# Kernel optimization log

Measured on AMD Instinct MI355X. Metric: run time of the kernel, lower is better.

Reference implementation:

```python
import jax, jax.numpy as jnp
import numpy as np

B, F, V, D = 16384, 16, 100000, 16  # batch, n_fields, vocab, embed_dim; dims = F*D = 256
EPS = 1e-5


def _bn(x, g, b):
    # torch.nn.BatchNorm1d in training mode: biased batch variance
    m = x.mean(0)
    v = x.var(0)
    return g * (x - m) * jax.lax.rsqrt(v + EPS) + b


def setup_inputs() -> dict:
    ks = iter(jax.random.split(jax.random.key(0), 40))

    def rn(shape, s=0.05):
        return jax.random.normal(next(ks), shape, jnp.float32) * s

    return {
        "feat_ids": jax.random.randint(next(ks), (B, F), 0, V, jnp.int32),
        "domain_ids": jax.random.randint(next(ks), (B,), 0, 3, jnp.int32),
        "emb": rn((F, V, D), 0.1),
        "hW0": rn((256, 128)), "hb0": jnp.zeros(128), "hg0": jnp.ones(128), "hbe0": jnp.zeros(128),
        "hW1": rn((128, 64)), "hb1": jnp.zeros(64), "hg1": jnp.ones(64), "hbe1": jnp.zeros(64),
        "hW2": rn((64, 1024)), "hb2": jnp.zeros(1024), "hg2": jnp.ones(1024), "hbe2": jnp.zeros(1024),
        "cw": rn((3, 256)), "cb": jnp.zeros((3, 256)),
        "mW0": rn((256, 512)), "mb0": jnp.zeros(512), "mg0": jnp.ones(512), "mbe0": jnp.zeros(512),
        "mW1": rn((512, 256)), "mb1": jnp.zeros(256), "mg1": jnp.ones(256), "mbe1": jnp.zeros(256),
        "u0": rn((256, 32)), "u1": rn((32, 32)), "v0": rn((32, 32)), "v1": rn((32, 256)),
        "ab0": jnp.zeros(32), "ab1": jnp.zeros(256),
        "gamma1": jnp.ones(256), "bias1": jnp.zeros(256),
        "lw": rn((512,)), "lb": jnp.zeros(1),
    }


def _forward(feat_ids, emb, hW0, hb0, hg0, hbe0, hW1, hb1, hg1, hbe1,
             hW2, hb2, hg2, hbe2, cw, cb, mW0, mb0, mg0, mbe0,
             mW1, mb1, mg1, mbe1, u0, u1, v0, v1, ab0, ab1,
             gamma1, bias1, lw, lb):
    b, f = feat_ids.shape
    # EmbeddingLayer(squeeze_dim=True): per-field lookup then concat -> [B, F*D]
    e = emb[jnp.arange(f)[None, :], feat_ids].reshape(b, -1)
    h = e
    for W, bb, g, be in ((hW0, hb0, hg0, hbe0), (hW1, hb1, hg1, hbe1), (hW2, hb2, hg2, hbe2)):
        h = jax.nn.relu(_bn(h @ W + bb, g, be))
    k = u1.shape[0]
    H = h.reshape(b, k, k)  # [B, k, k]
    # CrossNetwork: x_{l+1} = x0 * (x_l . w_l) + b_l + x_l
    x = e
    for i in range(cw.shape[0]):
        x = e * (x @ cw[i])[:, None] + cb[i] + x
    cn_out = x  # [B, 256]
    m = e
    for W, bb, g, be in ((mW0, mb0, mg0, mbe0), (mW1, mb1, mg1, mbe1)):
        m = jax.nn.relu(_bn(m @ W + bb, g, be))
    # hyper low-rank adapter: einsum('mi,bij,jn->bmn') applied lazily so the
    # [B,256,32] per-sample weight is never materialized (associativity)
    t = jax.nn.sigmoid(jnp.einsum('bi,bij->bj', m @ u0, H) @ v0 + ab0)   # [B, 32]
    t = jnp.einsum('bi,bij->bj', t @ u1, H) @ v1 + ab1                    # [B, 256]
    mu = t.mean(0)
    var = t.var(0, ddof=1)  # torch.var default is unbiased
    m = gamma1 * (t - mu) / jnp.sqrt(var + EPS) + bias1 + m  # norm + residual
    y = jnp.concatenate([cn_out, m], axis=1) @ lw + lb[0]     # LR head
    # Every domain branch computes identical values (shared weights, full-batch
    # input, dropout p=0), so the torch.where domain-select is the identity.
    return jax.nn.sigmoid(y)  # [B]


def reference(feat_ids, domain_ids, emb, hW0, hb0, hg0, hbe0, hW1, hb1, hg1, hbe1,
              hW2, hb2, hg2, hbe2, cw, cb, mW0, mb0, mg0, mbe0,
              mW1, mb1, mg1, mbe1, u0, u1, v0, v1, ab0, ab1,
              gamma1, bias1, lw, lb):
    return _forward(feat_ids, emb, hW0, hb0, hg0, hbe0, hW1, hb1, hg1, hbe1,
                    hW2, hb2, hg2, hbe2, cw, cb, mW0, mb0, mg0, mbe0,
                    mW1, mb1, mg1, mbe1, u0, u1, v0, v1, ab0, ab1,
                    gamma1, bias1, lw, lb)
```

## Files before the change

kernel.cpp:

```cpp
#include <hip/hip_runtime.h>

typedef unsigned short u16;
typedef __attribute__((ext_vector_type(8))) short bf16x8;
typedef __attribute__((ext_vector_type(4))) float f32x4;
#define BATCH 16384

__device__ __forceinline__ float b2f(u16 u){ unsigned int i=((unsigned int)u)<<16; float f; __builtin_memcpy(&f,&i,4); return f; }
__device__ __forceinline__ u16 f2b(float f){ unsigned int x; __builtin_memcpy(&x,&f,4); unsigned int r=(x + 0x7fffu + ((x>>16)&1u))>>16; return (u16)r; }

__global__ __launch_bounds__(256) void prep_kernel(float* __restrict__ S,
                                                   const float* __restrict__ hb0, const float* __restrict__ mb0,
                                                   float* __restrict__ catb,
                                                   const float* __restrict__ w0, const float* __restrict__ w1,
                                                   const float* __restrict__ w2, const float* __restrict__ w3,
                                                   const float* __restrict__ w4, const float* __restrict__ w5,
                                                   const float* __restrict__ w6,
                                                   u16* __restrict__ catWt, u16* __restrict__ t1,
                                                   u16* __restrict__ t2, u16* __restrict__ t4,
                                                   u16* __restrict__ t5, u16* __restrict__ t6,
                                                   const int* __restrict__ ids,
                                                   const float* __restrict__ emb,
                                                   u16* __restrict__ e){
  int blk = blockIdx.x;
  int tid = threadIdx.x;
  if (blk < 18){
    int i = blk*256 + tid;
    if (i < 4480) S[i] = 0.f;
  } else if (blk == 18){
    for (int i = tid; i < 640; i += 256) catb[i] = (i < 128) ? hb0[i] : mb0[i-128];
  } else if (blk < 1523){
    int c = blk - 19;
    if (c < 640){        int idx=c*256+tid;        int n=idx>>8, k=idx&255;
                         catWt[idx] = f2b(n<128 ? w0[k*128+n] : w3[k*512+(n-128)]); }
    else if (c < 672){   int idx=(c-640)*256+tid;  t1[idx]=f2b(w1[(idx%128)*64   + idx/128]); }
    else if (c < 928){   int idx=(c-672)*256+tid;  t2[idx]=f2b(w2[(idx%64)*1024  + idx/64]);  }
    else if (c < 1440){  int idx=(c-928)*256+tid;  t4[idx]=f2b(w4[(idx%512)*256  + idx/512]); }
    else if (c < 1472){  int idx=(c-1440)*256+tid; t5[idx]=f2b(w5[(idx%256)*32   + idx/256]); }
    else {               int idx=(c-1472)*256+tid; t6[idx]=f2b(w6[(idx%32)*256   + idx/32]);  }
  } else {
    int g = blk - 1523;
    int b = g*16 + (tid >> 4), f = tid & 15;
    int id = ids[b*16 + f];
    const float4* src = (const float4*)(emb + ((size_t)f*100000 + (size_t)id)*16);
    float4 v0 = src[0], v1 = src[1], v2 = src[2], v3 = src[3];
    u16 o[16] = { f2b(v0.x),f2b(v0.y),f2b(v0.z),f2b(v0.w), f2b(v1.x),f2b(v1.y),f2b(v1.z),f2b(v1.w),
                  f2b(v2.x),f2b(v2.y),f2b(v2.z),f2b(v2.w), f2b(v3.x),f2b(v3.y),f2b(v3.z),f2b(v3.w) };
    uint4 p0, p1; __builtin_memcpy(&p0, &o[0], 16); __builtin_memcpy(&p1, &o[8], 16);
    uint4* dst = (uint4*)(e + (size_t)b*256 + f*16);
    dst[0] = p0; dst[1] = p1;
  }
}

template<int BK>
__device__ __forceinline__ void gemm_body(const u16* __restrict__ A,
                                          const u16* __restrict__ Wt,
                                          const float* __restrict__ bias,
                                          u16* __restrict__ Ca,
                                          u16* __restrict__ Cb,
                                          int Nsplit,
                                          const float* __restrict__ asums,
                                          const float* __restrict__ asumsq,
                                          const float* __restrict__ ag,
                                          const float* __restrict__ abe,
                                          float* __restrict__ sums,
                                          float* __restrict__ sumsq,
                                          int N, int K, int n0, int m0,
                                          u16* lds, float* bnS, float* bnB){
  constexpr int STR = BK + 8;
  constexpr int EPT = BK/4;
  u16* As = lds;
  u16* Bs = lds + 64*STR;
  int tid = threadIdx.x;
  int lane = tid & 63, w = tid >> 6, quad = lane >> 4, m16 = lane & 15;
  int srow = tid >> 2, skoff = (tid & 3)*EPT;
  if (asums != nullptr){
    for (int k = tid; k < K; k += 256){
      float mean = asums[k] * (1.f/(float)BATCH);
      float var  = asumsq[k] * (1.f/(float)BATCH) - mean*mean;
      float sc   = ag[k] * rsqrtf(var + 1e-5f);
      bnS[k] = sc;
      bnB[k] = abe[k] - mean*sc;
    }
    __syncthreads();
  }
  f32x4 acc[4] = {};
  int ng = n0 + srow;
  uint4 a0, a1, b0, b1;
  {
    const u16* ap = A + (size_t)(m0+srow)*K + skoff;
    a0 = *(const uint4*)ap;
    if (EPT == 16) a1 = *(const uint4*)(ap + 8);
    if (ng < N){
      const u16* bp = Wt + (size_t)ng*K + skoff;
      b0 = *(const uint4*)bp;
      if (EPT == 16) b1 = *(const uint4*)(bp + 8);
    } else { b0 = make_uint4(0u,0u,0u,0u); b1 = b0; }
  }
  for (int k0 = 0; k0 < K; k0 += BK){
    u16 at[EPT];
    __builtin_memcpy(at, &a0, 16);
    if (EPT == 16) __builtin_memcpy(at+8, &a1, 16);
    if (asums != nullptr){
#pragma unroll
      for (int j=0;j<EPT;j++){
        float v = b2f(at[j]) * bnS[k0+skoff+j] + bnB[k0+skoff+j];
        at[j] = f2b(v > 0.f ? v : 0.f);
      }
    }
    uint4 s0, s1;
    __builtin_memcpy(&s0, at, 16);
    *(uint4*)&As[srow*STR + skoff] = s0;
    if (EPT == 16){ __builtin_memcpy(&s1, at+8, 16); *(uint4*)&As[srow*STR + skoff + 8] = s1; }
    *(uint4*)&Bs[srow*STR + skoff] = b0;
    if (EPT == 16) *(uint4*)&Bs[srow*STR + skoff + 8] = b1;
    if (k0 + BK < K){
      const u16* ap = A + (size_t)(m0+srow)*K + k0 + BK + skoff;
      a0 = *(const uint4*)ap;
      if (EPT == 16) a1 = *(const uint4*)(ap + 8);
      if (ng < N){
        const u16* bp = Wt + (size_t)ng*K + k0 + BK + skoff;
        b0 = *(const uint4*)bp;
        if (EPT == 16) b1 = *(const uint4*)(bp + 8);
      }
    }
    __syncthreads();
#pragma unroll
    for (int sub=0; sub<BK/32; sub++){
      bf16x8 bfrag = *(bf16x8*)&Bs[(w*16 + m16)*STR + sub*32 + quad*8];
#pragma unroll
      for (int mc=0;mc<4;mc++){
        bf16x8 afrag = *(bf16x8*)&As[(mc*16 + m16)*STR + sub*32 + quad*8];
        acc[mc] = __builtin_amdgcn_mfma_f32_16x16x32_bf16(afrag, bfrag, acc[mc], 0, 0, 0);
      }
    }
    __syncthreads();
  }
  int cw = n0 + w*16 + m16;
  float bvv = (bias != nullptr && cw < N) ? bias[cw] : 0.f;
  float cs = 0.f, cq = 0.f;
  u16* Cs = lds;
#pragma unroll
  for (int mc=0;mc<4;mc++)
#pragma unroll
    for (int r=0;r<4;r++){
      float v = acc[mc][r] + bvv;
      cs += v; cq += v*v;
      Cs[(mc*16 + quad*4 + r)*72 + w*16 + m16] = f2b(v);
    }
  if (sums != nullptr){
    cs += __shfl_xor(cs, 16, 64); cs += __shfl_xor(cs, 32, 64);
    cq += __shfl_xor(cq, 16, 64); cq += __shfl_xor(cq, 32, 64);
    if (quad == 0 && cw < N){ atomicAdd(&sums[cw], cs); atomicAdd(&sumsq[cw], cq); }
  }
  __syncthreads();
  int row = tid >> 2, c4 = (tid & 3)*16;
  int cg = n0 + c4;
  if (cg < N){
    u16* outp; int stride, colbase;
    if (Cb != nullptr && n0 >= Nsplit){ outp = Cb; stride = N - Nsplit; colbase = cg - Nsplit; }
    else if (Cb != nullptr){            outp = Ca; stride = Nsplit;     colbase = cg; }
    else {                              outp = Ca; stride = N;          colbase = cg; }
    uint4 p0 = *(uint4*)&Cs[row*72 + c4];
    uint4 p1 = *(uint4*)&Cs[row*72 + c4 + 8];
    *(uint4*)(outp + (size_t)(m0+row)*stride + colbase) = p0;
    *(uint4*)(outp + (size_t)(m0+row)*stride + colbase + 8) = p1;
  }
}

template<int BK>
__global__ __launch_bounds__(256) void gemm_mfma(const u16* __restrict__ A,
                                                 const u16* __restrict__ Wt,
                                                 const float* __restrict__ bias,
                                                 u16* __restrict__ Ca,
                                                 u16* __restrict__ Cb,
                                                 int Nsplit,
                                                 const float* __restrict__ asums,
                                                 const float* __restrict__ asumsq,
                                                 const float* __restrict__ ag,
                                                 const float* __restrict__ abe,
                                                 float* __restrict__ sums,
                                                 float* __restrict__ sumsq,
                                                 int N, int K){
  constexpr int STR = BK + 8;
  __shared__ u16 lds[64*STR*2];
  __shared__ float bnS[512], bnB[512];
  gemm_body<BK>(A, Wt, bias, Ca, Cb, Nsplit, asums, asumsq, ag, abe,
                sums, sumsq, N, K, blockIdx.x*64, blockIdx.y*64, lds, bnS, bnB);
}

__global__ __launch_bounds__(256) void gemm_dual(
    const u16* __restrict__ A1, const u16* __restrict__ Wt1, const float* __restrict__ b1,
    u16* __restrict__ C1,
    const float* __restrict__ as1, const float* __restrict__ aq1,
    const float* __restrict__ g1v, const float* __restrict__ be1,
    float* __restrict__ s1, float* __restrict__ q1, int N1, int K1, int nb1, int nblk1,
    const u16* __restrict__ A2, const u16* __restrict__ Wt2, const float* __restrict__ b2,
    u16* __restrict__ C2,
    const float* __restrict__ as2, const float* __restrict__ aq2,
    const float* __restrict__ g2v, const float* __restrict__ be2,
    float* __restrict__ s2, float* __restrict__ q2, int N2, int K2, int nblk2){
  constexpr int STR = 64 + 8;
  __shared__ u16 lds[64*STR*2];
  __shared__ float bnS[512], bnB[512];
  int blk = blockIdx.x;
  if (blk < nb1){
    int n0 = (blk % nblk1)*64, m0 = (blk / nblk1)*64;
    gemm_body<64>(A1, Wt1, b1, C1, nullptr, 0, as1, aq1, g1v, be1,
                  s1, q1, N1, K1, n0, m0, lds, bnS, bnB);
  } else {
    int q = blk - nb1;
    int n0 = (q % nblk2)*64, m0 = (q / nblk2)*64;
    gemm_body<64>(A2, Wt2, b2, C2, nullptr, 0, as2, aq2, g2v, be2,
                  s2, q2, N2, K2, n0, m0, lds, bnS, bnB);
  }
}

#define HSTR 1056
__global__ __launch_bounds__(512) void adapter_core(const u16* __restrict__ H,
                                                    const u16* __restrict__ Mout,
                                                    const u16* __restrict__ u0t,
                                                    const float* __restrict__ v0,
                                                    const float* __restrict__ u1,
                                                    const float* __restrict__ ab0,
                                                    const float* __restrict__ hsums,
                                                    const float* __restrict__ hsumsq,
                                                    const float* __restrict__ hg,
                                                    const float* __restrict__ hbe,
                                                    const float* __restrict__ msums,
                                                    const float* __restrict__ msumsq,
                                                    const float* __restrict__ mg,
                                                    const float* __restrict__ mbe,
                                                    u16* __restrict__ Z2){
  __shared__ __align__(16) u16 Hs[16*HSTR];
  __shared__ float bnS[1024], bnB[1024];
  __shared__ __align__(8) u16 v0s[1024], u1s[1024];
  __shared__ float mS[256], mB[256];
  __shared__ float PT[512], QS[512];
  __shared__ float ab0s[32];
  int tid = threadIdx.x;
  int r = tid >> 5, j = tid & 31;
  size_t row0 = (size_t)blockIdx.x * 16;
  u16* aS = Hs;

  for (int k = tid; k < 1024; k += 512){
    float mean = hsums[k] * (1.f/(float)BATCH);
    float var  = hsumsq[k] * (1.f/(float)BATCH) - mean*mean;
    float sc   = hg[k] * rsqrtf(var + 1e-5f);
    bnS[k] = sc; bnB[k] = hbe[k] - mean*sc;
  }
  if (tid < 256){
    float4 a = *(const float4*)(v0 + tid*4);
    ushort4 pa = { f2b(a.x), f2b(a.y), f2b(a.z), f2b(a.w) };
    *(ushort4*)&v0s[tid*4] = pa;
    float4 b4 = *(const float4*)(u1 + tid*4);
    ushort4 pb = { f2b(b4.x), f2b(b4.y), f2b(b4.z), f2b(b4.w) };
    *(ushort4*)&u1s[tid*4] = pb;
  } else {
    int c = tid - 256;
    float mean = msums[c] * (1.f/(float)BATCH);
    float var  = msumsq[c] * (1.f/(float)BATCH) - mean*mean;
    float sc   = mg[c] * rsqrtf(var + 1e-5f);
    mS[c] = sc; mB[c] = mbe[c] - mean*sc;
  }
  {
    int el = tid*8;
    uint4 mv = *(const uint4*)(Mout + row0*256 + el);
    *(uint4*)&aS[el] = mv;
  }
  if (tid < 32) ab0s[tid] = ab0[tid];
  __syncthreads();

  {
    int el = tid*8, col = el & 255;
    u16 mt[8]; __builtin_memcpy(mt, &aS[el], 16);
#pragma unroll
    for (int q=0;q<8;q++){
      float v = b2f(mt[q]) * mS[col+q] + mB[col+q];
      mt[q] = f2b(v > 0.f ? v : 0.f);
    }
    uint4 so; __builtin_memcpy(&so, mt, 16);
    *(uint4*)&aS[el] = so;
  }
  __syncthreads();

  {
    float acc = 0.f;
    for (int k8 = 0; k8 < 256; k8 += 8){
      uint4 vu = *(const uint4*)(u0t + j*256 + k8);
      uint4 va; __builtin_memcpy(&va, &aS[r*256 + k8], 16);
      u16 ta[8], tu[8]; __builtin_memcpy(ta, &va, 16); __builtin_memcpy(tu, &vu, 16);
#pragma unroll
      for (int q=0;q<8;q++) acc += b2f(ta[q]) * b2f(tu[q]);
    }
    PT[tid] = acc;
  }
  __syncthreads();

#pragma unroll
  for (int it=0; it<4; it++){
    int el = it*4096 + tid*8;
    int rr = el >> 10, col = el & 1023;
    uint4 hv = *(const uint4*)(H + row0*1024 + el);
    u16 ht[8]; __builtin_memcpy(ht, &hv, 16);
#pragma unroll
    for (int q=0;q<8;q++){
      float v = b2f(ht[q]) * bnS[col+q] + bnB[col+q];
      ht[q] = f2b(v > 0.f ? v : 0.f);
    }
    uint4 so; __builtin_memcpy(&so, ht, 16);
    *(uint4*)&Hs[rr*HSTR + col] = so;
  }
  __syncthreads();

  float acc = 0.f;
#pragma unroll
  for (int i=0;i<32;i++) acc += PT[r*32+i] * b2f(Hs[r*HSTR + i*32 + j]);
  QS[tid] = acc;
  __syncthreads();
  acc = ab0s[j];
#pragma unroll
  for (int i=0;i<32;i++) acc += QS[r*32+i] * b2f(v0s[i*32+j]);
  PT[tid] = 1.f / (1.f + __expf(-acc));
  __syncthreads();
  acc = 0.f;
#pragma unroll
  for (int i=0;i<32;i++) acc += PT[r*32+i] * b2f(u1s[i*32+j]);
  QS[tid] = acc;
  __syncthreads();
  acc = 0.f;
#pragma unroll
  for (int i=0;i<32;i++) acc += QS[r*32+i] * b2f(Hs[r*HSTR + i*32 + j]);
  Z2[(row0 + r)*32 + j] = f2b(acc);
}

__global__ __launch_bounds__(256) void final_kernel(const u16* __restrict__ e,
                                                    const float* __restrict__ cw,
                                                    const float* __restrict__ cb,
                                                    const u16* __restrict__ t,
                                                    const u16* __restrict__ mo,
                                                    const float* __restrict__ tsums,
                                                    const float* __restrict__ tsumsq,
                                                    const float* __restrict__ tg,
                                                    const float* __restrict__ tbe,
                                                    const float* __restrict__ msums,
                                                    const float* __restrict__ msumsq,
                                                    const float* __restrict__ mg,
                                                    const float* __restrict__ mbe,
                                                    const float* __restrict__ lw,
                                                    const float* __restrict__ lb,
                                                    float* __restrict__ out){
  __shared__ float tS[256], tB[256], mS[256], mB[256];
  int tid = threadIdx.x;
  {
    int c = tid;
    float mean = tsums[c] * (1.f/(float)BATCH);
    float var  = (tsumsq[c] - mean*mean*(float)BATCH) * (1.f/(float)(BATCH-1));
    float sc   = tg[c] * rsqrtf(var + 1e-5f);
    tS[c] = sc; tB[c] = tbe[c] - mean*sc;
    float mmean = msums[c] * (1.f/(float)BATCH);
    float mvar  = msumsq[c] * (1.f/(float)BATCH) - mmean*mmean;
    float msc   = mg[c] * rsqrtf(mvar + 1e-5f);
    mS[c] = msc; mB[c] = mbe[c] - mmean*msc;
  }
  __syncthreads();
  int wave = tid >> 6, lane = tid & 63;
  int b = blockIdx.x*4 + wave;
  int n4 = lane*4;
  ushort4 ev = *(const ushort4*)(e + (size_t)b*256 + n4);
  float ec[4] = { b2f(ev.x), b2f(ev.y), b2f(ev.z), b2f(ev.w) };
  float x[4]  = { ec[0], ec[1], ec[2], ec[3] };
  for (int i=0;i<3;i++){
    float p = 0.f;
#pragma unroll
    for (int q=0;q<4;q++) p += x[q] * cw[i*256 + n4 + q];
#pragma unroll
    for (int o=1;o<64;o<<=1) p += __shfl_xor(p, o, 64);
#pragma unroll
    for (int q=0;q<4;q++) x[q] = ec[q]*p + cb[i*256 + n4 + q] + x[q];
  }
  ushort4 tv = *(const ushort4*)(t  + (size_t)b*256 + n4);
  ushort4 mv = *(const ushort4*)(mo + (size_t)b*256 + n4);
  float ta[4] = { b2f(tv.x), b2f(tv.y), b2f(tv.z), b2f(tv.w) };
  float ma[4] = { b2f(mv.x), b2f(mv.y), b2f(mv.z), b2f(mv.w) };
  float p = 0.f;
#pragma unroll
  for (int q=0;q<4;q++){
    int n = n4 + q;
    p += x[q] * lw[n];
    float mr = ma[q]*mS[n] + mB[n];
    mr = mr > 0.f ? mr : 0.f;
    float mf = tS[n]*ta[q] + tB[n] + mr;
    p += mf * lw[256 + n];
  }
#pragma unroll
  for (int o=32;o>0;o>>=1) p += __shfl_down(p, o, 64);
  if (lane == 0){
    float y = p + lb[0];
    out[b] = 1.f / (1.f + __expf(-y));
  }
}

extern "C" void kernel_launch(void* const* d_in, const int* in_sizes, int n_in,
                              void* d_out, int out_size, void* d_ws, size_t ws_size,
                              hipStream_t stream) {
  const int B = BATCH;
  const int*   feat = (const int*)d_in[0];
  const float* emb  = (const float*)d_in[2];
  const float* hW0 = (const float*)d_in[3],  *hb0 = (const float*)d_in[4],  *hg0 = (const float*)d_in[5],  *hbe0 = (const float*)d_in[6];
  const float* hW1 = (const float*)d_in[7],  *hb1 = (const float*)d_in[8],  *hg1 = (const float*)d_in[9],  *hbe1 = (const float*)d_in[10];
  const float* hW2 = (const float*)d_in[11], *hb2 = (const float*)d_in[12], *hg2 = (const float*)d_in[13], *hbe2 = (const float*)d_in[14];
  const float* cw  = (const float*)d_in[15], *cb  = (const float*)d_in[16];
  const float* mW0 = (const float*)d_in[17], *mb0 = (const float*)d_in[18], *mg0 = (const float*)d_in[19], *mbe0 = (const float*)d_in[20];
  const float* mW1 = (const float*)d_in[21], *mb1 = (const float*)d_in[22], *mg1 = (const float*)d_in[23], *mbe1 = (const float*)d_in[24];
  const float* u0  = (const float*)d_in[25], *u1  = (const float*)d_in[26];
  const float* v0  = (const float*)d_in[27], *v1  = (const float*)d_in[28];
  const float* ab0 = (const float*)d_in[29], *ab1 = (const float*)d_in[30];
  const float* gamma1 = (const float*)d_in[31], *bias1 = (const float*)d_in[32];
  const float* lw  = (const float*)d_in[33], *lb = (const float*)d_in[34];
  float* out = (float*)d_out;

  char* base = (char*)d_ws;
  const size_t MB = 1024*1024;
  u16* H    = (u16*)(base);
  u16* e    = (u16*)(base + 32*MB);
  u16* Y0   = (u16*)(base + 40*MB);
  u16* Y1   = (u16*)(base + 44*MB);
  u16* M0   = (u16*)(base + 48*MB);
  u16* Mout = (u16*)(base + 64*MB);
  u16* T    = (u16*)(base + 72*MB);
  u16* Z2   = (u16*)(base + 80*MB);
  u16* catWt= (u16*)(base + 88*MB);
  u16* hW1t = catWt + 163840;
  u16* hW2t = hW1t + 8192;
  u16* mW1t = hW2t + 65536;
  u16* u0t  = mW1t + 131072;
  u16* v1t  = u0t + 8192;
  float* catb = (float*)(v1t + 8192);
  float* S    = catb + 640;

  prep_kernel<<<2547, 256, 0, stream>>>(S, hb0, mb0, catb,
                                        hW0, hW1, hW2, mW0, mW1, u0, v1,
                                        catWt, hW1t, hW2t, mW1t, u0t, v1t,
                                        feat, emb, e);

  gemm_mfma<64><<<dim3(10, B/64), 256, 0, stream>>>(e, catWt, catb, Y0, M0, 128,
      nullptr, nullptr, nullptr, nullptr, S+0, S+640, 640, 256);

  gemm_dual<<<1280, 256, 0, stream>>>(
      Y0, hW1t, hb1, Y1, S+0, S+640, hg0, hbe0, S+1280, S+1344, 64, 128, 256, 1,
      M0, mW1t, mb1, Mout, S+128, S+768, mg0, mbe0, S+3456, S+3712, 256, 512, 4);

  gemm_mfma<64><<<dim3(16, B/64), 256, 0, stream>>>(Y1, hW2t, hb2, H, nullptr, 0,
      S+1280, S+1344, hg1, hbe1, S+1408, S+2432, 1024, 64);

  adapter_core<<<B/16, 512, 0, stream>>>(H, Mout, u0t, v0, u1, ab0,
      S+1408, S+2432, hg2, hbe2, S+3456, S+3712, mg1, mbe1, Z2);
  gemm_mfma<32><<<dim3(4, B/64), 256, 0, stream>>>(Z2, v1t, ab1, T, nullptr, 0,
      nullptr, nullptr, nullptr, nullptr, S+3968, S+4224, 256, 32);

  final_kernel<<<B/4, 256, 0, stream>>>(e, cw, cb, T, Mout,
      S+3968, S+4224, gamma1, bias1,
      S+3456, S+3712, mg1, mbe1, lw, lb, out);
}
```

Measured before the change: 324.3 us.

## Switch main GEMMs to 128x128 tiles with 4x4 MFMA per wave

Adds a 128x128-tile GEMM body where each wave computes a 64x64 sub-tile (4x4 MFMA 16x16x32 fragments) and output goes through LDS for coalesced stores. The first, dual and hyper-net-layer-2 GEMMs use it, which raises operand reuse and roughly quarters the block count. The BN scale/shift setup now runs after the first global loads are issued, so that latency overlaps. The trade-off is higher register and LDS use per block and fewer blocks, which lowers occupancy and may underfill the GPU. Tiles that fall past N (e.g., N=64 in a 128 tile) waste MFMA work.

```diff
diff --git a/kernel.cpp b/kernel.cpp
--- a/kernel.cpp
+++ b/kernel.cpp
@@ -73,16 +73,6 @@
   int tid = threadIdx.x;
   int lane = tid & 63, w = tid >> 6, quad = lane >> 4, m16 = lane & 15;
   int srow = tid >> 2, skoff = (tid & 3)*EPT;
-  if (asums != nullptr){
-    for (int k = tid; k < K; k += 256){
-      float mean = asums[k] * (1.f/(float)BATCH);
-      float var  = asumsq[k] * (1.f/(float)BATCH) - mean*mean;
-      float sc   = ag[k] * rsqrtf(var + 1e-5f);
-      bnS[k] = sc;
-      bnB[k] = abe[k] - mean*sc;
-    }
-    __syncthreads();
-  }
   f32x4 acc[4] = {};
   int ng = n0 + srow;
   uint4 a0, a1, b0, b1;
@@ -95,6 +85,16 @@
       b0 = *(const uint4*)bp;
       if (EPT == 16) b1 = *(const uint4*)(bp + 8);
     } else { b0 = make_uint4(0u,0u,0u,0u); b1 = b0; }
+  }
+  if (asums != nullptr){
+    for (int k = tid; k < K; k += 256){
+      float mean = asums[k] * (1.f/(float)BATCH);
+      float var  = asumsq[k] * (1.f/(float)BATCH) - mean*mean;
+      float sc   = ag[k] * rsqrtf(var + 1e-5f);
+      bnS[k] = sc;
+      bnB[k] = abe[k] - mean*sc;
+    }
+    __syncthreads();
   }
   for (int k0 = 0; k0 < K; k0 += BK){
     u16 at[EPT];
@@ -182,36 +182,188 @@
                                                  float* __restrict__ sumsq,
                                                  int N, int K){
   constexpr int STR = BK + 8;
-  __shared__ u16 lds[64*STR*2];
+  __shared__ __align__(16) u16 lds[64*STR*2];
   __shared__ float bnS[512], bnB[512];
   gemm_body<BK>(A, Wt, bias, Ca, Cb, Nsplit, asums, asumsq, ag, abe,
                 sums, sumsq, N, K, blockIdx.x*64, blockIdx.y*64, lds, bnS, bnB);
 }
 
-__global__ __launch_bounds__(256) void gemm_dual(
+__device__ __forceinline__ void gemm128_body(const u16* __restrict__ A,
+                                             const u16* __restrict__ Wt,
+                                             const float* __restrict__ bias,
+                                             u16* __restrict__ Ca,
+                                             u16* __restrict__ Cb,
+                                             int Nsplit,
+                                             const float* __restrict__ asums,
+                                             const float* __restrict__ asumsq,
+                                             const float* __restrict__ ag,
+                                             const float* __restrict__ abe,
+                                             float* __restrict__ sums,
+                                             float* __restrict__ sumsq,
+                                             int N, int K, int n0, int m0,
+                                             u16* lds, float* bnS, float* bnB){
+  constexpr int BK = 64, STR = 72, CSTR = 136;
+  u16* As = lds;
+  u16* Bs = lds + 128*STR;
+  int tid = threadIdx.x;
+  int lane = tid & 63, w = tid >> 6, quad = lane >> 4, m16 = lane & 15;
+  int wr = (w >> 1)*64, wc = (w & 1)*64;
+  int srow = tid >> 1, skoff = (tid & 1)*32;
+  int ng = n0 + srow;
+  uint4 a0,a1,a2,a3, b0,b1,b2,b3;
+  {
+    const u16* ap = A + (size_t)(m0+srow)*K + skoff;
+    a0 = *(const uint4*)ap;       a1 = *(const uint4*)(ap+8);
+    a2 = *(const uint4*)(ap+16);  a3 = *(const uint4*)(ap+24);
+    if (ng < N){
+      const u16* bp = Wt + (size_t)ng*K + skoff;
+      b0 = *(const uint4*)bp;       b1 = *(const uint4*)(bp+8);
+      b2 = *(const uint4*)(bp+16);  b3 = *(const uint4*)(bp+24);
+    } else { b0 = make_uint4(0u,0u,0u,0u); b1 = b0; b2 = b0; b3 = b0; }
+  }
+  if (asums != nullptr){
+    for (int k = tid; k < K; k += 256){
+      float mean = asums[k] * (1.f/(float)BATCH);
+      float var  = asumsq[k] * (1.f/(float)BATCH) - mean*mean;
+      float sc   = ag[k] * rsqrtf(var + 1e-5f);
+      bnS[k] = sc;
+      bnB[k] = abe[k] - mean*sc;
+    }
+    __syncthreads();
+  }
+  f32x4 acc[4][4] = {};
+  for (int k0 = 0; k0 < K; k0 += BK){
+    u16 at[32];
+    __builtin_memcpy(at,    &a0, 16); __builtin_memcpy(at+8,  &a1, 16);
+    __builtin_memcpy(at+16, &a2, 16); __builtin_memcpy(at+24, &a3, 16);
+    if (asums != nullptr){
+#pragma unroll
+      for (int j=0;j<32;j++){
+        float v = b2f(at[j]) * bnS[k0+skoff+j] + bnB[k0+skoff+j];
+        at[j] = f2b(v > 0.f ? v : 0.f);
+      }
+    }
+    uint4 s0,s1,s2,s3;
+    __builtin_memcpy(&s0, at,    16); __builtin_memcpy(&s1, at+8,  16);
+    __builtin_memcpy(&s2, at+16, 16); __builtin_memcpy(&s3, at+24, 16);
+    uint4* adst = (uint4*)&As[srow*STR + skoff];
+    adst[0]=s0; adst[1]=s1; adst[2]=s2; adst[3]=s3;
+    uint4* bdst = (uint4*)&Bs[srow*STR + skoff];
+    bdst[0]=b0; bdst[1]=b1; bdst[2]=b2; bdst[3]=b3;
+    if (k0 + BK < K){
+      const u16* ap = A + (size_t)(m0+srow)*K + k0 + BK + skoff;
+      a0 = *(const uint4*)ap;       a1 = *(const uint4*)(ap+8);
+      a2 = *(const uint4*)(ap+16);  a3 = *(const uint4*)(ap+24);
+      if (ng < N){
+        const u16* bp = Wt + (size_t)ng*K + k0 + BK + skoff;
+        b0 = *(const uint4*)bp;       b1 = *(const uint4*)(bp+8);
+        b2 = *(const uint4*)(bp+16);  b3 = *(const uint4*)(bp+24);
+      }
+    }
+    __syncthreads();
+#pragma unroll
+    for (int sub=0; sub<2; sub++){
+      bf16x8 bfr[4], afr[4];
+#pragma unroll
+      for (int nc=0;nc<4;nc++) bfr[nc] = *(bf16x8*)&Bs[(wc + nc*16 + m16)*STR + sub*32 + quad*8];
+#pragma unroll
+      for (int mc=0;mc<4;mc++) afr[mc] = *(bf16x8*)&As[(wr + mc*16 + m16)*STR + sub*32 + quad*8];
+#pragma unroll
+      for (int mc=0;mc<4;mc++)
+#pragma unroll
+        for (int nc=0;nc<4;nc++)
+          acc[mc][nc] = __builtin_amdgcn_mfma_f32_16x16x32_bf16(afr[mc], bfr[nc], acc[mc][nc], 0, 0, 0);
+    }
+    __syncthreads();
+  }
+  u16* Cs = lds;
+  float cs[4], cq[4];
+#pragma unroll
+  for (int nc=0;nc<4;nc++){
+    int cwn = n0 + wc + nc*16 + m16;
+    float bvv = (bias != nullptr && cwn < N) ? bias[cwn] : 0.f;
+    cs[nc] = 0.f; cq[nc] = 0.f;
+#pragma unroll
+    for (int mc=0;mc<4;mc++)
+#pragma unroll
+      for (int r=0;r<4;r++){
+        float v = acc[mc][nc][r] + bvv;
+        cs[nc] += v; cq[nc] += v*v;
+        Cs[(wr + mc*16 + quad*4 + r)*CSTR + wc + nc*16 + m16] = f2b(v);
+      }
+  }
+  if (sums != nullptr){
+#pragma unroll
+    for (int nc=0;nc<4;nc++){
+      float s = cs[nc], q = cq[nc];
+      s += __shfl_xor(s, 16, 64); s += __shfl_xor(s, 32, 64);
+      q += __shfl_xor(q, 16, 64); q += __shfl_xor(q, 32, 64);
+      int cwn = n0 + wc + nc*16 + m16;
+      if (quad == 0 && cwn < N){ atomicAdd(&sums[cwn], s); atomicAdd(&sumsq[cwn], q); }
+    }
+  }
+  __syncthreads();
+#pragma unroll
+  for (int p=0;p<2;p++){
+    int row = (tid>>2) + p*64;
+#pragma unroll
+    for (int qb=0;qb<2;qb++){
+      int cb16 = (tid & 3)*16 + qb*64;
+      int cg = n0 + cb16;
+      if (cg < N){
+        u16* outp; int stride, colbase;
+        if (Cb != nullptr && cg >= Nsplit){ outp = Cb; stride = N - Nsplit; colbase = cg - Nsplit; }
+        else if (Cb != nullptr){            outp = Ca; stride = Nsplit;     colbase = cg; }
+        else {                              outp = Ca; stride = N;          colbase = cg; }
+        uint4 p0 = *(uint4*)&Cs[row*CSTR + cb16];
+        uint4 p1 = *(uint4*)&Cs[row*CSTR + cb16 + 8];
+        *(uint4*)(outp + (size_t)(m0+row)*stride + colbase) = p0;
+        *(uint4*)(outp + (size_t)(m0+row)*stride + colbase + 8) = p1;
+      }
+    }
+  }
+}
+
+__global__ __launch_bounds__(256) void gemm128(const u16* __restrict__ A,
+                                               const u16* __restrict__ Wt,
+                                               const float* __restrict__ bias,
+                                               u16* __restrict__ Ca,
+                                               u16* __restrict__ Cb,
+                                               int Nsplit,
+                                               const float* __restrict__ asums,
+                                               const float* __restrict__ asumsq,
+                                               const float* __restrict__ ag,
+                                               const float* __restrict__ abe,
+                                               float* __restrict__ sums,
+                                               float* __restrict__ sumsq,
+                                               int N, int K){
+  __shared__ __align__(16) u16 lds[128*72*2];
+  __shared__ float bnS[512], bnB[512];
+  gemm128_body(A, Wt, bias, Ca, Cb, Nsplit, asums, asumsq, ag, abe,
+               sums, sumsq, N, K, blockIdx.x*128, blockIdx.y*128, lds, bnS, bnB);
+}
+
+__global__ __launch_bounds__(256) void gemm_dual128(
     const u16* __restrict__ A1, const u16* __restrict__ Wt1, const float* __restrict__ b1,
     u16* __restrict__ C1,
     const float* __restrict__ as1, const float* __restrict__ aq1,
     const float* __restrict__ g1v, const float* __restrict__ be1,
-    float* __restrict__ s1, float* __restrict__ q1, int N1, int K1, int nb1, int nblk1,
+    float* __restrict__ s1, float* __restrict__ q1, int N1, int K1, int nb1,
     const u16* __restrict__ A2, const u16* __restrict__ Wt2, const float* __restrict__ b2,
     u16* __restrict__ C2,
     const float* __restrict__ as2, const float* __restrict__ aq2,
     const float* __restrict__ g2v, const float* __restrict__ be2,
     float* __restrict__ s2, float* __restrict__ q2, int N2, int K2, int nblk2){
-  constexpr int STR = 64 + 8;
-  __shared__ u16 lds[64*STR*2];
+  __shared__ __align__(16) u16 lds[128*72*2];
   __shared__ float bnS[512], bnB[512];
   int blk = blockIdx.x;
   if (blk < nb1){
-    int n0 = (blk % nblk1)*64, m0 = (blk / nblk1)*64;
-    gemm_body<64>(A1, Wt1, b1, C1, nullptr, 0, as1, aq1, g1v, be1,
-                  s1, q1, N1, K1, n0, m0, lds, bnS, bnB);
+    gemm128_body(A1, Wt1, b1, C1, nullptr, 0, as1, aq1, g1v, be1,
+                 s1, q1, N1, K1, 0, blk*128, lds, bnS, bnB);
   } else {
     int q = blk - nb1;
-    int n0 = (q % nblk2)*64, m0 = (q / nblk2)*64;
-    gemm_body<64>(A2, Wt2, b2, C2, nullptr, 0, as2, aq2, g2v, be2,
-                  s2, q2, N2, K2, n0, m0, lds, bnS, bnB);
+    gemm128_body(A2, Wt2, b2, C2, nullptr, 0, as2, aq2, g2v, be2,
+                 s2, q2, N2, K2, (q % nblk2)*128, (q / nblk2)*128, lds, bnS, bnB);
   }
 }
 
@@ -443,14 +595,14 @@
                                         catWt, hW1t, hW2t, mW1t, u0t, v1t,
                                         feat, emb, e);
 
-  gemm_mfma<64><<<dim3(10, B/64), 256, 0, stream>>>(e, catWt, catb, Y0, M0, 128,
+  gemm128<<<dim3(5, B/128), 256, 0, stream>>>(e, catWt, catb, Y0, M0, 128,
       nullptr, nullptr, nullptr, nullptr, S+0, S+640, 640, 256);
 
-  gemm_dual<<<1280, 256, 0, stream>>>(
-      Y0, hW1t, hb1, Y1, S+0, S+640, hg0, hbe0, S+1280, S+1344, 64, 128, 256, 1,
-      M0, mW1t, mb1, Mout, S+128, S+768, mg0, mbe0, S+3456, S+3712, 256, 512, 4);
-
-  gemm_mfma<64><<<dim3(16, B/64), 256, 0, stream>>>(Y1, hW2t, hb2, H, nullptr, 0,
+  gemm_dual128<<<128 + 256, 256, 0, stream>>>(
+      Y0, hW1t, hb1, Y1, S+0, S+640, hg0, hbe0, S+1280, S+1344, 64, 128, 128,
+      M0, mW1t, mb1, Mout, S+128, S+768, mg0, mbe0, S+3456, S+3712, 256, 512, 2);
+
+  gemm128<<<dim3(8, B/128), 256, 0, stream>>>(Y1, hW2t, hb2, H, nullptr, 0,
       S+1280, S+1344, hg1, hbe1, S+1408, S+2432, 1024, 64);
 
   adapter_core<<<B/16, 512, 0, stream>>>(H, Mout, u0t, v0, u1, ab0,
```

Result: slower. 337.9 us (+4.2%).

## Derive T batch statistics from Z Gram matrix and recompute T in final kernel

Applied to the files above, without the earlier changes.

Removes the separate Z2·v1 GEMM that wrote the [B,256] T tensor. adapter_core now accumulates the 32x32 Gram matrix and column sums of Z through atomics, and a one-block kernel turns these into the per-channel mean and variance of T algebraically. final_kernel recomputes each block's T rows on the fly with MFMA from Z2 and v1t. This saves the T round-trip through memory and one launch, at the cost of many atomics, a serial single-block kernel, and variance computed as E[x²]-mean², which is less numerically stable.

```diff
diff --git a/kernel.cpp b/kernel.cpp
--- a/kernel.cpp
+++ b/kernel.cpp
@@ -9,6 +9,7 @@
 __device__ __forceinline__ u16 f2b(float f){ unsigned int x; __builtin_memcpy(&x,&f,4); unsigned int r=(x + 0x7fffu + ((x>>16)&1u))>>16; return (u16)r; }
 
 __global__ __launch_bounds__(256) void prep_kernel(float* __restrict__ S,
+                                                   float* __restrict__ Z,
                                                    const float* __restrict__ hb0, const float* __restrict__ mb0,
                                                    float* __restrict__ catb,
                                                    const float* __restrict__ w0, const float* __restrict__ w1,
@@ -26,10 +27,13 @@
   if (blk < 18){
     int i = blk*256 + tid;
     if (i < 4480) S[i] = 0.f;
-  } else if (blk == 18){
+  } else if (blk < 25){
+    int i = (blk-18)*256 + tid;
+    if (i < 1568) Z[i] = 0.f;
+  } else if (blk == 25){
     for (int i = tid; i < 640; i += 256) catb[i] = (i < 128) ? hb0[i] : mb0[i-128];
-  } else if (blk < 1523){
-    int c = blk - 19;
+  } else if (blk < 1530){
+    int c = blk - 26;
     if (c < 640){        int idx=c*256+tid;        int n=idx>>8, k=idx&255;
                          catWt[idx] = f2b(n<128 ? w0[k*128+n] : w3[k*512+(n-128)]); }
     else if (c < 672){   int idx=(c-640)*256+tid;  t1[idx]=f2b(w1[(idx%128)*64   + idx/128]); }
@@ -38,7 +42,7 @@
     else if (c < 1472){  int idx=(c-1440)*256+tid; t5[idx]=f2b(w5[(idx%256)*32   + idx/256]); }
     else {               int idx=(c-1472)*256+tid; t6[idx]=f2b(w6[(idx%32)*256   + idx/32]);  }
   } else {
-    int g = blk - 1523;
+    int g = blk - 1530;
     int b = g*16 + (tid >> 4), f = tid & 15;
     int id = ids[b*16 + f];
     const float4* src = (const float4*)(emb + ((size_t)f*100000 + (size_t)id)*16);
@@ -182,7 +186,7 @@
                                                  float* __restrict__ sumsq,
                                                  int N, int K){
   constexpr int STR = BK + 8;
-  __shared__ u16 lds[64*STR*2];
+  __shared__ __align__(16) u16 lds[64*STR*2];
   __shared__ float bnS[512], bnB[512];
   gemm_body<BK>(A, Wt, bias, Ca, Cb, Nsplit, asums, asumsq, ag, abe,
                 sums, sumsq, N, K, blockIdx.x*64, blockIdx.y*64, lds, bnS, bnB);
@@ -200,7 +204,7 @@
     const float* __restrict__ g2v, const float* __restrict__ be2,
     float* __restrict__ s2, float* __restrict__ q2, int N2, int K2, int nblk2){
   constexpr int STR = 64 + 8;
-  __shared__ u16 lds[64*STR*2];
+  __shared__ __align__(16) u16 lds[64*STR*2];
   __shared__ float bnS[512], bnB[512];
   int blk = blockIdx.x;
   if (blk < nb1){
@@ -230,7 +234,9 @@
                                                     const float* __restrict__ msumsq,
                                                     const float* __restrict__ mg,
                                                     const float* __restrict__ mbe,
-                                                    u16* __restrict__ Z2){
+                                                    u16* __restrict__ Z2,
+                                                    float* __restrict__ gramZ,
+                                                    float* __restrict__ colsumZ){
   __shared__ __align__(16) u16 Hs[16*HSTR];
   __shared__ float bnS[1024], bnB[1024];
   __shared__ __align__(8) u16 v0s[1024], u1s[1024];
@@ -330,41 +336,120 @@
   acc = 0.f;
 #pragma unroll
   for (int i=0;i<32;i++) acc += QS[r*32+i] * b2f(Hs[r*HSTR + i*32 + j]);
-  Z2[(row0 + r)*32 + j] = f2b(acc);
+  u16 zb = f2b(acc);
+  Z2[(row0 + r)*32 + j] = zb;
+  PT[tid] = b2f(zb);
+  __syncthreads();
+
+  if (tid < 32){
+    float c = 0.f;
+#pragma unroll
+    for (int rr=0; rr<16; rr++) c += PT[rr*32 + tid];
+    atomicAdd(&colsumZ[tid], c);
+  }
+#pragma unroll
+  for (int e2 = tid; e2 < 1024; e2 += 512){
+    int gi = e2 >> 5, gj = e2 & 31;
+    float g = 0.f;
+#pragma unroll
+    for (int rr=0; rr<16; rr++) g += PT[rr*32 + gi] * PT[rr*32 + gj];
+    atomicAdd(&gramZ[e2], g);
+  }
+}
+
+__global__ __launch_bounds__(256) void ttable_kernel(const float* __restrict__ gramZ,
+                                                     const float* __restrict__ colsumZ,
+                                                     const u16* __restrict__ v1t,
+                                                     const float* __restrict__ ab1,
+                                                     const float* __restrict__ tg,
+                                                     const float* __restrict__ tbe,
+                                                     float* __restrict__ tSg,
+                                                     float* __restrict__ tBg){
+  __shared__ float Gs[1024], cS[32];
+  int tid = threadIdx.x;
+  for (int i = tid; i < 1024; i += 256) Gs[i] = gramZ[i];
+  if (tid < 32) cS[tid] = colsumZ[tid];
+  __syncthreads();
+  float v[32];
+  {
+    const uint4* vr = (const uint4*)(v1t + tid*32);
+    uint4 q0 = vr[0], q1 = vr[1], q2 = vr[2], q3 = vr[3];
+    u16 tv[32];
+    __builtin_memcpy(tv,    &q0, 16); __builtin_memcpy(tv+8,  &q1, 16);
+    __builtin_memcpy(tv+16, &q2, 16); __builtin_memcpy(tv+24, &q3, 16);
+#pragma unroll
+    for (int k=0;k<32;k++) v[k] = b2f(tv[k]);
+  }
+  float sv = 0.f;
+#pragma unroll
+  for (int k=0;k<32;k++) sv += cS[k]*v[k];
+  float qf = 0.f;
+#pragma unroll
+  for (int i=0;i<32;i++){
+    float u = 0.f;
+#pragma unroll
+    for (int jj=0;jj<32;jj++) u += Gs[i*32+jj]*v[jj];
+    qf += u*v[i];
+  }
+  float a = ab1[tid];
+  float tsum = sv + (float)BATCH*a;
+  float tsq  = qf + 2.f*a*sv + (float)BATCH*a*a;
+  float mean = tsum * (1.f/(float)BATCH);
+  float var  = (tsq - mean*mean*(float)BATCH) * (1.f/(float)(BATCH-1));
+  float sc   = tg[tid] * rsqrtf(var + 1e-5f);
+  tSg[tid] = sc;
+  tBg[tid] = tbe[tid] - mean*sc;
 }
 
 __global__ __launch_bounds__(256) void final_kernel(const u16* __restrict__ e,
                                                     const float* __restrict__ cw,
                                                     const float* __restrict__ cb,
-                                                    const u16* __restrict__ t,
-                                                    const u16* __restrict__ mo,
-                                                    const float* __restrict__ tsums,
-                                                    const float* __restrict__ tsumsq,
-                                                    const float* __restrict__ tg,
-                                                    const float* __restrict__ tbe,
+                                                    const u16* __restrict__ z2g,
+                                                    const u16* __restrict__ v1t,
+                                                    const float* __restrict__ ab1,
+                                                    const float* __restrict__ tSg,
+                                                    const float* __restrict__ tBg,
                                                     const float* __restrict__ msums,
                                                     const float* __restrict__ msumsq,
                                                     const float* __restrict__ mg,
                                                     const float* __restrict__ mbe,
+                                                    const u16* __restrict__ mo,
                                                     const float* __restrict__ lw,
                                                     const float* __restrict__ lb,
                                                     float* __restrict__ out){
   __shared__ float tS[256], tB[256], mS[256], mB[256];
+  __shared__ __align__(8) u16 Ts[1024];
   int tid = threadIdx.x;
   {
     int c = tid;
-    float mean = tsums[c] * (1.f/(float)BATCH);
-    float var  = (tsumsq[c] - mean*mean*(float)BATCH) * (1.f/(float)(BATCH-1));
-    float sc   = tg[c] * rsqrtf(var + 1e-5f);
-    tS[c] = sc; tB[c] = tbe[c] - mean*sc;
+    tS[c] = tSg[c]; tB[c] = tBg[c];
     float mmean = msums[c] * (1.f/(float)BATCH);
     float mvar  = msumsq[c] * (1.f/(float)BATCH) - mmean*mmean;
     float msc   = mg[c] * rsqrtf(mvar + 1e-5f);
     mS[c] = msc; mB[c] = mbe[c] - mmean*msc;
   }
-  __syncthreads();
   int wave = tid >> 6, lane = tid & 63;
   int b = blockIdx.x*4 + wave;
+  if (wave == 0){
+    int m16 = lane & 15, quad = lane >> 4;
+    size_t bb = (size_t)blockIdx.x * 4;
+    bf16x8 afrag = *(const bf16x8*)(z2g + (bb + (size_t)(m16 & 3))*32 + quad*8);
+    f32x4 zero4 = {0.f, 0.f, 0.f, 0.f};
+    f32x4 tacc[16];
+#pragma unroll
+    for (int t=0;t<16;t++){
+      bf16x8 bfrag = *(const bf16x8*)(v1t + (size_t)(t*16 + m16)*32 + quad*8);
+      tacc[t] = __builtin_amdgcn_mfma_f32_16x16x32_bf16(afrag, bfrag, zero4, 0, 0, 0);
+    }
+    if (quad == 0){
+#pragma unroll
+      for (int t=0;t<16;t++){
+        float bv = ab1[t*16 + m16];
+#pragma unroll
+        for (int rr=0;rr<4;rr++) Ts[rr*256 + t*16 + m16] = f2b(tacc[t][rr] + bv);
+      }
+    }
+  }
   int n4 = lane*4;
   ushort4 ev = *(const ushort4*)(e + (size_t)b*256 + n4);
   float ec[4] = { b2f(ev.x), b2f(ev.y), b2f(ev.z), b2f(ev.w) };
@@ -378,7 +463,8 @@
 #pragma unroll
     for (int q=0;q<4;q++) x[q] = ec[q]*p + cb[i*256 + n4 + q] + x[q];
   }
-  ushort4 tv = *(const ushort4*)(t  + (size_t)b*256 + n4);
+  __syncthreads();
+  ushort4 tv = *(const ushort4*)&Ts[wave*256 + n4];
   ushort4 mv = *(const ushort4*)(mo + (size_t)b*256 + n4);
   float ta[4] = { b2f(tv.x), b2f(tv.y), b2f(tv.z), b2f(tv.w) };
   float ma[4] = { b2f(mv.x), b2f(mv.y), b2f(mv.z), b2f(mv.w) };
@@ -427,7 +513,7 @@
   u16* Y1   = (u16*)(base + 44*MB);
   u16* M0   = (u16*)(base + 48*MB);
   u16* Mout = (u16*)(base + 64*MB);
-  u16* T    = (u16*)(base + 72*MB);
+  float* ZZ = (float*)(base + 72*MB);
   u16* Z2   = (u16*)(base + 80*MB);
   u16* catWt= (u16*)(base + 88*MB);
   u16* hW1t = catWt + 163840;
@@ -438,7 +524,12 @@
   float* catb = (float*)(v1t + 8192);
   float* S    = catb + 640;
 
-  prep_kernel<<<2547, 256, 0, stream>>>(S, hb0, mb0, catb,
+  float* gramZ   = ZZ;
+  float* colsumZ = ZZ + 1024;
+  float* tSg     = ZZ + 1056;
+  float* tBg     = ZZ + 1312;
+
+  prep_kernel<<<2554, 256, 0, stream>>>(S, ZZ, hb0, mb0, catb,
                                         hW0, hW1, hW2, mW0, mW1, u0, v1,
                                         catWt, hW1t, hW2t, mW1t, u0t, v1t,
                                         feat, emb, e);
@@ -454,11 +545,10 @@
       S+1280, S+1344, hg1, hbe1, S+1408, S+2432, 1024, 64);
 
   adapter_core<<<B/16, 512, 0, stream>>>(H, Mout, u0t, v0, u1, ab0,
-      S+1408, S+2432, hg2, hbe2, S+3456, S+3712, mg1, mbe1, Z2);
-  gemm_mfma<32><<<dim3(4, B/64), 256, 0, stream>>>(Z2, v1t, ab1, T, nullptr, 0,
-      nullptr, nullptr, nullptr, nullptr, S+3968, S+4224, 256, 32);
-
-  final_kernel<<<B/4, 256, 0, stream>>>(e, cw, cb, T, Mout,
-      S+3968, S+4224, gamma1, bias1,
-      S+3456, S+3712, mg1, mbe1, lw, lb, out);
-}
+      S+1408, S+2432, hg2, hbe2, S+3456, S+3712, mg1, mbe1, Z2, gramZ, colsumZ);
+
+  ttable_kernel<<<1, 256, 0, stream>>>(gramZ, colsumZ, v1t, ab1, gamma1, bias1, tSg, tBg);
+
+  final_kernel<<<B/4, 256, 0, stream>>>(e, cw, cb, Z2, v1t, ab1, tSg, tBg,
+      S+3456, S+3712, mg1, mbe1, Mout, lw, lb, out);
+}
```

Measured after the change: 353.9 us. 9.1% more time.

## Precompute BN tables in a separate kernel, prefetch H, and drop adapter barriers

Applied to the files above, without the earlier changes.

The per-column BatchNorm scale/shift tables for H and Mout are computed once in a new tiny kernel, instead of being recomputed by every adapter_core and final_kernel block. adapter_core now issues its H tile loads at the start of the kernel so they overlap the M-normalization work. It also reads the scale/shift values straight from global memory and drops several __syncthreads. Those barriers are removed on the assumption that each 32-lane row group's LDS producers and consumers sit in the same 64-wide wavefront. The change adds one kernel launch, and it relies on wave-level ordering for correctness.

```diff
diff --git a/kernel.cpp b/kernel.cpp
--- a/kernel.cpp
+++ b/kernel.cpp
@@ -182,7 +182,7 @@
                                                  float* __restrict__ sumsq,
                                                  int N, int K){
   constexpr int STR = BK + 8;
-  __shared__ u16 lds[64*STR*2];
+  __shared__ __align__(16) u16 lds[64*STR*2];
   __shared__ float bnS[512], bnB[512];
   gemm_body<BK>(A, Wt, bias, Ca, Cb, Nsplit, asums, asumsq, ag, abe,
                 sums, sumsq, N, K, blockIdx.x*64, blockIdx.y*64, lds, bnS, bnB);
@@ -200,7 +200,7 @@
     const float* __restrict__ g2v, const float* __restrict__ be2,
     float* __restrict__ s2, float* __restrict__ q2, int N2, int K2, int nblk2){
   constexpr int STR = 64 + 8;
-  __shared__ u16 lds[64*STR*2];
+  __shared__ __align__(16) u16 lds[64*STR*2];
   __shared__ float bnS[512], bnB[512];
   int blk = blockIdx.x;
   if (blk < nb1){
@@ -215,6 +215,33 @@
   }
 }
 
+__global__ __launch_bounds__(256) void tables_kernel(const float* __restrict__ hsums,
+                                                     const float* __restrict__ hsumsq,
+                                                     const float* __restrict__ hg,
+                                                     const float* __restrict__ hbe,
+                                                     const float* __restrict__ msums,
+                                                     const float* __restrict__ msumsq,
+                                                     const float* __restrict__ mg,
+                                                     const float* __restrict__ mbe,
+                                                     float* __restrict__ hSg,
+                                                     float* __restrict__ hBg,
+                                                     float* __restrict__ mSg,
+                                                     float* __restrict__ mBg){
+  int i = blockIdx.x*256 + threadIdx.x;
+  if (i < 1024){
+    float mean = hsums[i] * (1.f/(float)BATCH);
+    float var  = hsumsq[i] * (1.f/(float)BATCH) - mean*mean;
+    float sc   = hg[i] * rsqrtf(var + 1e-5f);
+    hSg[i] = sc; hBg[i] = hbe[i] - mean*sc;
+    if (i < 256){
+      float mmean = msums[i] * (1.f/(float)BATCH);
+      float mvar  = msumsq[i] * (1.f/(float)BATCH) - mmean*mmean;
+      float msc   = mg[i] * rsqrtf(mvar + 1e-5f);
+      mSg[i] = msc; mBg[i] = mbe[i] - mmean*msc;
+    }
+  }
+}
+
 #define HSTR 1056
 __global__ __launch_bounds__(512) void adapter_core(const u16* __restrict__ H,
                                                     const u16* __restrict__ Mout,
@@ -222,19 +249,13 @@
                                                     const float* __restrict__ v0,
                                                     const float* __restrict__ u1,
                                                     const float* __restrict__ ab0,
-                                                    const float* __restrict__ hsums,
-                                                    const float* __restrict__ hsumsq,
-                                                    const float* __restrict__ hg,
-                                                    const float* __restrict__ hbe,
-                                                    const float* __restrict__ msums,
-                                                    const float* __restrict__ msumsq,
-                                                    const float* __restrict__ mg,
-                                                    const float* __restrict__ mbe,
+                                                    const float* __restrict__ hSg,
+                                                    const float* __restrict__ hBg,
+                                                    const float* __restrict__ mSg,
+                                                    const float* __restrict__ mBg,
                                                     u16* __restrict__ Z2){
   __shared__ __align__(16) u16 Hs[16*HSTR];
-  __shared__ float bnS[1024], bnB[1024];
   __shared__ __align__(8) u16 v0s[1024], u1s[1024];
-  __shared__ float mS[256], mB[256];
   __shared__ float PT[512], QS[512];
   __shared__ float ab0s[32];
   int tid = threadIdx.x;
@@ -242,11 +263,27 @@
   size_t row0 = (size_t)blockIdx.x * 16;
   u16* aS = Hs;
 
-  for (int k = tid; k < 1024; k += 512){
-    float mean = hsums[k] * (1.f/(float)BATCH);
-    float var  = hsumsq[k] * (1.f/(float)BATCH) - mean*mean;
-    float sc   = hg[k] * rsqrtf(var + 1e-5f);
-    bnS[k] = sc; bnB[k] = hbe[k] - mean*sc;
+  const u16* Hb = H + row0*1024 + tid*8;
+  uint4 h0 = *(const uint4*)(Hb);
+  uint4 h1 = *(const uint4*)(Hb + 4096);
+  uint4 h2 = *(const uint4*)(Hb + 8192);
+  uint4 h3 = *(const uint4*)(Hb + 12288);
+
+  {
+    int el = tid*8, col = el & 255;
+    uint4 mv = *(const uint4*)(Mout + row0*256 + el);
+    float4 s0 = *(const float4*)(mSg + col), s1 = *(const float4*)(mSg + col + 4);
+    float4 bb0 = *(const float4*)(mBg + col), bb1 = *(const float4*)(mBg + col + 4);
+    float sv[8] = { s0.x,s0.y,s0.z,s0.w, s1.x,s1.y,s1.z,s1.w };
+    float bv[8] = { bb0.x,bb0.y,bb0.z,bb0.w, bb1.x,bb1.y,bb1.z,bb1.w };
+    u16 mt[8]; __builtin_memcpy(mt, &mv, 16);
+#pragma unroll
+    for (int q=0;q<8;q++){
+      float v = b2f(mt[q]) * sv[q] + bv[q];
+      mt[q] = f2b(v > 0.f ? v : 0.f);
+    }
+    uint4 so; __builtin_memcpy(&so, mt, 16);
+    *(uint4*)&aS[el] = so;
   }
   if (tid < 256){
     float4 a = *(const float4*)(v0 + tid*4);
@@ -255,33 +292,9 @@
     float4 b4 = *(const float4*)(u1 + tid*4);
     ushort4 pb = { f2b(b4.x), f2b(b4.y), f2b(b4.z), f2b(b4.w) };
     *(ushort4*)&u1s[tid*4] = pb;
-  } else {
-    int c = tid - 256;
-    float mean = msums[c] * (1.f/(float)BATCH);
-    float var  = msumsq[c] * (1.f/(float)BATCH) - mean*mean;
-    float sc   = mg[c] * rsqrtf(var + 1e-5f);
-    mS[c] = sc; mB[c] = mbe[c] - mean*sc;
-  }
-  {
-    int el = tid*8;
-    uint4 mv = *(const uint4*)(Mout + row0*256 + el);
-    *(uint4*)&aS[el] = mv;
-  }
-  if (tid < 32) ab0s[tid] = ab0[tid];
-  __syncthreads();
-
-  {
-    int el = tid*8, col = el & 255;
-    u16 mt[8]; __builtin_memcpy(mt, &aS[el], 16);
-#pragma unroll
-    for (int q=0;q<8;q++){
-      float v = b2f(mt[q]) * mS[col+q] + mB[col+q];
-      mt[q] = f2b(v > 0.f ? v : 0.f);
-    }
-    uint4 so; __builtin_memcpy(&so, mt, 16);
-    *(uint4*)&aS[el] = so;
-  }
-  __syncthreads();
+  } else if (tid < 288){
+    ab0s[tid-256] = ab0[tid-256];
+  }
 
   {
     float acc = 0.f;
@@ -300,11 +313,15 @@
   for (int it=0; it<4; it++){
     int el = it*4096 + tid*8;
     int rr = el >> 10, col = el & 1023;
-    uint4 hv = *(const uint4*)(H + row0*1024 + el);
+    uint4 hv = (it==0)?h0:(it==1)?h1:(it==2)?h2:h3;
+    float4 s0 = *(const float4*)(hSg + col), s1 = *(const float4*)(hSg + col + 4);
+    float4 bb0 = *(const float4*)(hBg + col), bb1 = *(const float4*)(hBg + col + 4);
+    float sv[8] = { s0.x,s0.y,s0.z,s0.w, s1.x,s1.y,s1.z,s1.w };
+    float bv[8] = { bb0.x,bb0.y,bb0.z,bb0.w, bb1.x,bb1.y,bb1.z,bb1.w };
     u16 ht[8]; __builtin_memcpy(ht, &hv, 16);
 #pragma unroll
     for (int q=0;q<8;q++){
-      float v = b2f(ht[q]) * bnS[col+q] + bnB[col+q];
+      float v = b2f(ht[q]) * sv[q] + bv[q];
       ht[q] = f2b(v > 0.f ? v : 0.f);
     }
     uint4 so; __builtin_memcpy(&so, ht, 16);
@@ -316,17 +333,14 @@
 #pragma unroll
   for (int i=0;i<32;i++) acc += PT[r*32+i] * b2f(Hs[r*HSTR + i*32 + j]);
   QS[tid] = acc;
-  __syncthreads();
   acc = ab0s[j];
 #pragma unroll
   for (int i=0;i<32;i++) acc += QS[r*32+i] * b2f(v0s[i*32+j]);
   PT[tid] = 1.f / (1.f + __expf(-acc));
-  __syncthreads();
   acc = 0.f;
 #pragma unroll
   for (int i=0;i<32;i++) acc += PT[r*32+i] * b2f(u1s[i*32+j]);
   QS[tid] = acc;
-  __syncthreads();
   acc = 0.f;
 #pragma unroll
   for (int i=0;i<32;i++) acc += QS[r*32+i] * b2f(Hs[r*HSTR + i*32 + j]);
@@ -342,10 +356,8 @@
                                                     const float* __restrict__ tsumsq,
                                                     const float* __restrict__ tg,
                                                     const float* __restrict__ tbe,
-                                                    const float* __restrict__ msums,
-                                                    const float* __restrict__ msumsq,
-                                                    const float* __restrict__ mg,
-                                                    const float* __restrict__ mbe,
+                                                    const float* __restrict__ mSg,
+                                                    const float* __restrict__ mBg,
                                                     const float* __restrict__ lw,
                                                     const float* __restrict__ lb,
                                                     float* __restrict__ out){
@@ -357,10 +369,7 @@
     float var  = (tsumsq[c] - mean*mean*(float)BATCH) * (1.f/(float)(BATCH-1));
     float sc   = tg[c] * rsqrtf(var + 1e-5f);
     tS[c] = sc; tB[c] = tbe[c] - mean*sc;
-    float mmean = msums[c] * (1.f/(float)BATCH);
-    float mvar  = msumsq[c] * (1.f/(float)BATCH) - mmean*mmean;
-    float msc   = mg[c] * rsqrtf(mvar + 1e-5f);
-    mS[c] = msc; mB[c] = mbe[c] - mmean*msc;
+    mS[c] = mSg[c]; mB[c] = mBg[c];
   }
   __syncthreads();
   int wave = tid >> 6, lane = tid & 63;
@@ -429,6 +438,7 @@
   u16* Mout = (u16*)(base + 64*MB);
   u16* T    = (u16*)(base + 72*MB);
   u16* Z2   = (u16*)(base + 80*MB);
+  float* TZ = (float*)(base + 82*MB);
   u16* catWt= (u16*)(base + 88*MB);
   u16* hW1t = catWt + 163840;
   u16* hW2t = hW1t + 8192;
@@ -438,6 +448,11 @@
   float* catb = (float*)(v1t + 8192);
   float* S    = catb + 640;
 
+  float* hSg = TZ;
+  float* hBg = TZ + 1024;
+  float* mSg = TZ + 2048;
+  float* mBg = TZ + 2304;
+
   prep_kernel<<<2547, 256, 0, stream>>>(S, hb0, mb0, catb,
                                         hW0, hW1, hW2, mW0, mW1, u0, v1,
                                         catWt, hW1t, hW2t, mW1t, u0t, v1t,
@@ -453,12 +468,15 @@
   gemm_mfma<64><<<dim3(16, B/64), 256, 0, stream>>>(Y1, hW2t, hb2, H, nullptr, 0,
       S+1280, S+1344, hg1, hbe1, S+1408, S+2432, 1024, 64);
 
+  tables_kernel<<<4, 256, 0, stream>>>(S+1408, S+2432, hg2, hbe2,
+                                       S+3456, S+3712, mg1, mbe1,
+                                       hSg, hBg, mSg, mBg);
+
   adapter_core<<<B/16, 512, 0, stream>>>(H, Mout, u0t, v0, u1, ab0,
-      S+1408, S+2432, hg2, hbe2, S+3456, S+3712, mg1, mbe1, Z2);
+      hSg, hBg, mSg, mBg, Z2);
   gemm_mfma<32><<<dim3(4, B/64), 256, 0, stream>>>(Z2, v1t, ab1, T, nullptr, 0,
       nullptr, nullptr, nullptr, nullptr, S+3968, S+4224, 256, 32);
 
   final_kernel<<<B/4, 256, 0, stream>>>(e, cw, cb, T, Mout,
-      S+3968, S+4224, gamma1, bias1,
-      S+3456, S+3712, mg1, mbe1, lw, lb, out);
-}
+      S+3968, S+4224, gamma1, bias1, mSg, mBg, lw, lb, out);
+}
```

Result: no change. 327.5 us (+1.0%).
